# Kernel tuning notes

Measured on AMD Instinct MI355X. Metric: run time of the kernel, lower is better.

The kernel has to match this reference:

```python
import jax, jax.numpy as jnp
import numpy as np

DIM = 3456      # visual_dim
E = 1024        # embed_dim = dim_head*heads = 128*8
H = 8
D = E // H
LN_EPS = 1e-5


def _mlp(x, w1, b1, w2, b2):
    # nn.Sequential(Linear, GELU(exact), Linear)
    h = jax.nn.gelu(x @ w1.T + b1, approximate=False)
    return h @ w2.T + b2


def _ln(x, g, b):
    m = jnp.mean(x, axis=-1, keepdims=True)
    v = jnp.mean((x - m) ** 2, axis=-1, keepdims=True)
    return (x - m) * jax.lax.rsqrt(v + LN_EPS) * g + b


def setup_inputs() -> dict:
    key = jax.random.key(0)
    ks = jax.random.split(key, 24)
    std = 0.02
    d = {"x": jax.random.normal(ks[0], (5, 729, DIM), dtype=jnp.float32)}
    i = 1
    for name in ("q", "k", "v"):
        d[f"{name}_w1"] = std * jax.random.normal(ks[i], (E, DIM), dtype=jnp.float32); i += 1
        d[f"{name}_b1"] = jnp.zeros((E,), jnp.float32)
        d[f"{name}_w2"] = std * jax.random.normal(ks[i], (E, E), dtype=jnp.float32); i += 1
        d[f"{name}_b2"] = jnp.zeros((E,), jnp.float32)
        d[f"ln_{name}_g"] = jnp.ones((E,), jnp.float32)
        d[f"ln_{name}_b"] = jnp.zeros((E,), jnp.float32)
    d["in_proj_w"] = std * jax.random.normal(ks[i], (3 * E, E), dtype=jnp.float32); i += 1
    d["in_proj_b"] = jnp.zeros((3 * E,), jnp.float32)
    d["out_proj_w"] = std * jax.random.normal(ks[i], (E, E), dtype=jnp.float32); i += 1
    d["out_proj_b"] = jnp.zeros((E,), jnp.float32)
    d["to_out_w"] = std * jax.random.normal(ks[i], (DIM, E), dtype=jnp.float32)
    return d


def reference(x,
              q_w1, q_b1, q_w2, q_b2, ln_q_g, ln_q_b,
              k_w1, k_b1, k_w2, k_b2, ln_k_g, ln_k_b,
              v_w1, v_b1, v_w2, v_b2, ln_v_g, ln_v_b,
              in_proj_w, in_proj_b, out_proj_w, out_proj_b, to_out_w):
    t, hw, c = x.shape
    # spatial_temporal pattern: x_multi = x, no interpolation.
    # q/k/v: MLP -> LN -> permute(1,0,2) -> divide_feature -> flatten.
    # divide_feature is a pure permutation of tokens; all tokens end up in a
    # single (L, 1, E) attention, so full attention over the flattened
    # (hw, t) token order computes the identical result.
    q = _ln(_mlp(x, q_w1, q_b1, q_w2, q_b2), ln_q_g, ln_q_b)  # (t, hw, E)
    k = _ln(_mlp(x, k_w1, k_b1, k_w2, k_b2), ln_k_g, ln_k_b)
    v = _ln(_mlp(x, v_w1, v_b1, v_w2, v_b2), ln_v_g, ln_v_b)
    L = t * hw
    q = q.transpose(1, 0, 2).reshape(L, E)  # (hw*t, E), (h,w,t)-major order
    k = k.transpose(1, 0, 2).reshape(L, E)
    v = v.transpose(1, 0, 2).reshape(L, E)
    # nn.MultiheadAttention with packed in_proj
    qp = (q @ in_proj_w[:E].T + in_proj_b[:E]).reshape(L, H, D)
    kp = (k @ in_proj_w[E:2 * E].T + in_proj_b[E:2 * E]).reshape(L, H, D)
    vp = (v @ in_proj_w[2 * E:].T + in_proj_b[2 * E:]).reshape(L, H, D)
    scale = 1.0 / jnp.sqrt(jnp.asarray(D, q.dtype))
    scores = jnp.einsum('qhd,khd->hqk', qp, kp) * scale  # (H, L, L)
    attn = jax.nn.softmax(scores, axis=-1)
    o = jnp.einsum('hqk,khd->qhd', attn, vp).reshape(L, E)
    o = o @ out_proj_w.T + out_proj_b
    o = o.reshape(hw, t, E).transpose(1, 0, 2)  # (t, hw, E)
    out = o @ to_out_w.T                         # (t, hw, c)
    return x + out
```

## Files before the change

### kernel.cpp

```cpp
#include <hip/hip_runtime.h>
#include <hip/hip_bf16.h>

#define L_TOK 3645
#define MP    3712
#define DIMV  3456
#define EDIM  1024

typedef __attribute__((ext_vector_type(8))) short bf8;
typedef __attribute__((ext_vector_type(4))) short s4v;
typedef __attribute__((ext_vector_type(4))) float f4;

__device__ __forceinline__ short f2b(float f) {
  union { float f; unsigned u; } v; v.f = f;
  unsigned r = v.u + 0x7fffu + ((v.u >> 16) & 1u);
  return (short)(r >> 16);
}
__device__ __forceinline__ float b2f(short s) {
  union { unsigned u; float f; } v; v.u = ((unsigned)(unsigned short)s) << 16;
  return v.f;
}
__device__ __forceinline__ void gld16(const void* g, void* l) {
  __builtin_amdgcn_global_load_lds(
      (const __attribute__((address_space(1))) void*)(unsigned long long)g,
      (__attribute__((address_space(3))) void*)(unsigned)(unsigned long long)l,
      16, 0, 0);
}

struct CvtArgs {
  const float *s0, *s1, *s2, *s3, *s4, *s5, *s6, *s7;
  short *d0, *d1, *d2, *d3, *d4, *d5, *d6, *d7;
};
#define SB0 3207168
#define SB1 4091904
#define SB2 4976640
#define SB3 5861376
#define SB4 6123520
#define SB5 6385664
#define SB6 6647808
#define SB7 7532544
__global__ __launch_bounds__(256) void k_cvtall(CvtArgs a) {
  int i = blockIdx.x * 256 + threadIdx.x;
  if (i >= SB7) return;
  const float* src; short* dst; int j;
  if (i < SB0) {
    j = i; src = a.s0; dst = a.d0;
    s4v o; o[0] = 0; o[1] = 0; o[2] = 0; o[3] = 0;
    if (j < 3149280) {
      float4 v = ((const float4*)src)[j];
      o[0] = f2b(v.x); o[1] = f2b(v.y); o[2] = f2b(v.z); o[3] = f2b(v.w);
    }
    ((s4v*)dst)[j] = o;
    return;
  }
  else if (i < SB1) { j = i - SB0; src = a.s1; dst = a.d1; }
  else if (i < SB2) { j = i - SB1; src = a.s2; dst = a.d2; }
  else if (i < SB3) { j = i - SB2; src = a.s3; dst = a.d3; }
  else if (i < SB4) { j = i - SB3; src = a.s4; dst = a.d4; }
  else if (i < SB5) { j = i - SB4; src = a.s5; dst = a.d5; }
  else if (i < SB6) { j = i - SB5; src = a.s6; dst = a.d6; }
  else              { j = i - SB6; src = a.s7; dst = a.d7; }
  float4 v = ((const float4*)src)[j];
  s4v o; o[0] = f2b(v.x); o[1] = f2b(v.y); o[2] = f2b(v.z); o[3] = f2b(v.w);
  ((s4v*)dst)[j] = o;
}

__global__ __launch_bounds__(256)
void k_cvtwp(const float* __restrict__ src, short* __restrict__ dst,
             const float* __restrict__ g0, const float* __restrict__ g1,
             const float* __restrict__ g2) {
  int i = blockIdx.x * 256 + threadIdx.x;
  if (i >= 786432) return;
  int flat = i * 4;
  int k = flat & 1023;
  int z = flat >> 20;
  const float* g = (z == 0) ? g0 : (z == 1 ? g1 : g2);
  float4 v = ((const float4*)src)[i];
  float4 gv = *(const float4*)&g[k];
  s4v o; o[0] = f2b(v.x * gv.x); o[1] = f2b(v.y * gv.y);
  o[2] = f2b(v.z * gv.z); o[3] = f2b(v.w * gv.w);
  ((s4v*)dst)[i] = o;
}

__global__ __launch_bounds__(256)
void k_cvt_t(const float* __restrict__ src, short* __restrict__ dst, int n) {
  __shared__ float T[64][65];
  const int bi = blockIdx.x * 64, bj = blockIdx.y * 64;
  const int tx = threadIdx.x & 63, ty = threadIdx.x >> 6;
#pragma unroll
  for (int r = 0; r < 64; r += 4)
    T[r + ty][tx] = src[(long)(bj + r + ty) * n + bi + tx];
  __syncthreads();
#pragma unroll
  for (int r = 0; r < 64; r += 4)
    dst[(long)(bi + r + ty) * n + bj + tx] = f2b(T[tx][r + ty]);
}

__global__ __launch_bounds__(256)
void k_bvec(const float* __restrict__ wt, const float* __restrict__ opb,
            float* __restrict__ bp) {
  const int n = blockIdx.x * 4 + (threadIdx.x >> 6);
  const int lane = threadIdx.x & 63;
  const float* row = wt + (long)n * 1024;
  float s = 0.f;
  for (int k = lane * 4; k < 1024; k += 256) {
    float4 w = *(const float4*)&row[k];
    float4 b = *(const float4*)&opb[k];
    s += w.x * b.x + w.y * b.y + w.z * b.z + w.w * b.w;
  }
#pragma unroll
  for (int off = 1; off < 64; off <<= 1) s += __shfl_xor(s, off);
  if (lane == 0) bp[n] = s;
}

__global__ __launch_bounds__(256)
void k_cvec(const float* __restrict__ wp,
            const float* g0, const float* g1, const float* g2,
            const float* b0, const float* b1, const float* b2,
            const float* __restrict__ ipb,
            float* __restrict__ c1, float* __restrict__ cb2) {
  const int z = blockIdx.y;
  const int n = blockIdx.x * 4 + (threadIdx.x >> 6);
  const int lane = threadIdx.x & 63;
  const float* g  = (z == 0) ? g0 : (z == 1 ? g1 : g2);
  const float* lb = (z == 0) ? b0 : (z == 1 ? b1 : b2);
  const float* row = wp + ((long)z * 1024 + n) * 1024;
  float s1 = 0.f, s2 = 0.f;
  for (int k = lane * 4; k < 1024; k += 256) {
    float4 w = *(const float4*)&row[k];
    float4 gv = *(const float4*)&g[k];
    float4 bv = *(const float4*)&lb[k];
    s1 += w.x * gv.x + w.y * gv.y + w.z * gv.z + w.w * gv.w;
    s2 += w.x * bv.x + w.y * bv.y + w.z * bv.z + w.w * bv.w;
  }
#pragma unroll
  for (int off = 1; off < 64; off <<= 1) {
    s1 += __shfl_xor(s1, off); s2 += __shfl_xor(s2, off);
  }
  if (lane == 0) { c1[z * 1024 + n] = s1; cb2[z * 1024 + n] = s2 + ipb[z * 1024 + n]; }
}

__global__ __launch_bounds__(256)
void k_stats(const short* __restrict__ aln, float2* __restrict__ st) {
  const int z = blockIdx.y;
  const int row = blockIdx.x * 4 + (threadIdx.x >> 6);
  const int lane = threadIdx.x & 63;
  const short* a = aln + ((long)z * MP + row) * EDIM;
  float s = 0.f, q = 0.f;
  for (int k = lane * 4; k < 1024; k += 256) {
    s4v v = *(const s4v*)&a[k];
#pragma unroll
    for (int e = 0; e < 4; ++e) { float f = b2f(v[e]); s += f; q += f * f; }
  }
#pragma unroll
  for (int off = 1; off < 64; off <<= 1) {
    s += __shfl_xor(s, off); q += __shfl_xor(q, off);
  }
  if (lane == 0) {
    float m = s * (1.f / 1024.f);
    float var = q * (1.f / 1024.f) - m * m;
    float2 o; o.x = m; o.y = rsqrtf(var + 1e-5f);
    st[(long)z * MP + row] = o;
  }
}

#define GM_GELU   0
#define GM_BIAS   1
#define GM_QSCALE 2
#define GM_RESID  3
#define GM_PLAIN  4

template<int MODE>
__global__ __launch_bounds__(256)
void k_gemm(const short* __restrict__ A, long sA,
            const short* __restrict__ B, long sB,
            const float* __restrict__ bias0, const float* __restrict__ bias1,
            const float* __restrict__ bias2,
            void* __restrict__ Cout, long sC,
            int N, int K, const float* __restrict__ resid)
{
  __shared__ short As[2][128 * 32];
  __shared__ short Bs[2][128 * 32];
  const int tid  = threadIdx.x;
  const int z    = blockIdx.z;
  const int nwg  = gridDim.x * gridDim.y;
  const int orig = blockIdx.y * gridDim.x + blockIdx.x;
  const int qq   = nwg >> 3, rr = nwg & 7;
  const int xcd  = orig & 7, ofs = orig >> 3;
  const int swz  = (xcd < rr ? xcd * (qq + 1) : rr * (qq + 1) + (xcd - rr) * qq) + ofs;
  const int brow = (swz / gridDim.x) * 128;
  const int bcol = (swz % gridDim.x) * 128;

  const short* Ab = A + (long)z * sA;
  const short* Bb = B + (long)z * sB;
  const float* bias = (z == 0) ? bias0 : (z == 1 ? bias1 : bias2);

  const int wave = tid >> 6, lane = tid & 63;
  const int lg = lane >> 4, lc = lane & 15;
  const int m0 = (wave >> 1) * 64, n0 = (wave & 1) * 64;

  const int r0 = tid >> 2, seg = tid & 3;
  const int r1 = r0 + 64;
  const int so0 = (seg ^ ((r0 >> 1) & 3)) * 8;
  const int so1 = (seg ^ ((r1 >> 1) & 3)) * 8;
  const short* pA0 = Ab + (long)(brow + r0) * K + so0;
  const short* pA1 = Ab + (long)(brow + r1) * K + so1;
  const short* pB0 = Bb + (long)(bcol + r0) * K + so0;
  const short* pB1 = Bb + (long)(bcol + r1) * K + so1;

  f4 acc[4][4];
  f4 zero = {0.f, 0.f, 0.f, 0.f};
#pragma unroll
  for (int i = 0; i < 4; ++i)
#pragma unroll
    for (int j = 0; j < 4; ++j) acc[i][j] = zero;

  auto STAGE = [&](int buf) {
    gld16(pA0, &As[buf][tid * 8]);
    gld16(pA1, &As[buf][(tid + 256) * 8]);
    gld16(pB0, &Bs[buf][tid * 8]);
    gld16(pB1, &Bs[buf][(tid + 256) * 8]);
    pA0 += 32; pA1 += 32; pB0 += 32; pB1 += 32;
  };

  const int NT = K >> 5;
  STAGE(0);
  for (int t = 0; t < NT; ++t) {
    const int buf = t & 1;
    asm volatile("s_waitcnt vmcnt(0)" ::: "memory");
    __builtin_amdgcn_sched_barrier(0);
    __builtin_amdgcn_s_barrier();
    if (t + 1 < NT) STAGE((t + 1) & 1);
    const short* Al = &As[buf][0];
    const short* Bl = &Bs[buf][0];
    bf8 af[4], bfr[4];
#pragma unroll
    for (int mi = 0; mi < 4; ++mi) {
      int r = m0 + mi * 16 + lc;
      af[mi] = *(const bf8*)&Al[r * 32 + ((lg ^ ((r >> 1) & 3)) * 8)];
    }
#pragma unroll
    for (int ni = 0; ni < 4; ++ni) {
      int r = n0 + ni * 16 + lc;
      bfr[ni] = *(const bf8*)&Bl[r * 32 + ((lg ^ ((r >> 1) & 3)) * 8)];
    }
    __builtin_amdgcn_s_setprio(1);
#pragma unroll
    for (int mi = 0; mi < 4; ++mi)
#pragma unroll
      for (int ni = 0; ni < 4; ++ni)
        acc[mi][ni] = __builtin_amdgcn_mfma_f32_16x16x32_bf16(af[mi], bfr[ni], acc[mi][ni], 0, 0, 0);
    __builtin_amdgcn_s_setprio(0);
    __builtin_amdgcn_sched_barrier(0);
  }

  if (MODE == GM_RESID) {
    float* C = (float*)Cout;
#pragma unroll
    for (int ni = 0; ni < 4; ++ni) {
      int col = bcol + n0 + ni * 16 + lc;
      float bv = bias[col];
#pragma unroll
      for (int mi = 0; mi < 4; ++mi)
#pragma unroll
        for (int r = 0; r < 4; ++r) {
          int row = brow + m0 + mi * 16 + lg * 4 + r;
          if (row < L_TOK)
            C[(long)row * N + col] = acc[mi][ni][r] + bv + resid[(long)row * N + col];
        }
    }
  } else {
    short* C = (short*)Cout + (long)z * sC;
    const float alpha = (MODE == GM_QSCALE && z == 0) ? 0.08838834764831845f : 1.0f;
#pragma unroll
    for (int ni = 0; ni < 4; ++ni) {
      int col = bcol + n0 + ni * 16 + lc;
      float bv = 0.f;
      if (MODE != GM_PLAIN) bv = bias[col];
#pragma unroll
      for (int mi = 0; mi < 4; ++mi)
#pragma unroll
        for (int r = 0; r < 4; ++r) {
          int row = brow + m0 + mi * 16 + lg * 4 + r;
          float v = acc[mi][ni][r] + bv;
          if (MODE == GM_GELU) v = 0.5f * v * (1.f + erff(v * 0.70710678118654752f));
          v *= alpha;
          C[(long)row * EDIM + col] = f2b(v);
        }
    }
  }
}

__global__ __launch_bounds__(256)
void k_gemmln(const short* __restrict__ A, long sA,
              const short* __restrict__ B, long sB,
              const float2* __restrict__ st,
              const float* __restrict__ c1, const float* __restrict__ cb2,
              short* __restrict__ Cout, long sC)
{
  __shared__ short As[2][128 * 32];
  __shared__ short Bs[2][128 * 32];
  const int tid  = threadIdx.x;
  const int z    = blockIdx.z;
  const int K    = EDIM;
  const int nwg  = gridDim.x * gridDim.y;
  const int orig = blockIdx.y * gridDim.x + blockIdx.x;
  const int qq   = nwg >> 3, rr = nwg & 7;
  const int xcd  = orig & 7, ofs = orig >> 3;
  const int swz  = (xcd < rr ? xcd * (qq + 1) : rr * (qq + 1) + (xcd - rr) * qq) + ofs;
  const int brow = (swz / gridDim.x) * 128;
  const int bcol = (swz % gridDim.x) * 128;

  const short* Ab = A + (long)z * sA;
  const short* Bb = B + (long)z * sB;

  const int wave = tid >> 6, lane = tid & 63;
  const int lg = lane >> 4, lc = lane & 15;
  const int m0 = (wave >> 1) * 64, n0 = (wave & 1) * 64;

  const int r0 = tid >> 2, seg = tid & 3;
  const int r1 = r0 + 64;
  const int so0 = (seg ^ ((r0 >> 1) & 3)) * 8;
  const int so1 = (seg ^ ((r1 >> 1) & 3)) * 8;
  const short* pA0 = Ab + (long)(brow + r0) * K + so0;
  const short* pA1 = Ab + (long)(brow + r1) * K + so1;
  const short* pB0 = Bb + (long)(bcol + r0) * K + so0;
  const short* pB1 = Bb + (long)(bcol + r1) * K + so1;

  f4 acc[4][4];
  f4 zero = {0.f, 0.f, 0.f, 0.f};
#pragma unroll
  for (int i = 0; i < 4; ++i)
#pragma unroll
    for (int j = 0; j < 4; ++j) acc[i][j] = zero;

  auto STAGE = [&](int buf) {
    gld16(pA0, &As[buf][tid * 8]);
    gld16(pA1, &As[buf][(tid + 256) * 8]);
    gld16(pB0, &Bs[buf][tid * 8]);
    gld16(pB1, &Bs[buf][(tid + 256) * 8]);
    pA0 += 32; pA1 += 32; pB0 += 32; pB1 += 32;
  };

  const int NT = K >> 5;
  STAGE(0);
  for (int t = 0; t < NT; ++t) {
    const int buf = t & 1;
    asm volatile("s_waitcnt vmcnt(0)" ::: "memory");
    __builtin_amdgcn_sched_barrier(0);
    __builtin_amdgcn_s_barrier();
    if (t + 1 < NT) STAGE((t + 1) & 1);
    const short* Al = &As[buf][0];
    const short* Bl = &Bs[buf][0];
    bf8 af[4], bfr[4];
#pragma unroll
    for (int mi = 0; mi < 4; ++mi) {
      int r = m0 + mi * 16 + lc;
      af[mi] = *(const bf8*)&Al[r * 32 + ((lg ^ ((r >> 1) & 3)) * 8)];
    }
#pragma unroll
    for (int ni = 0; ni < 4; ++ni) {
      int r = n0 + ni * 16 + lc;
      bfr[ni] = *(const bf8*)&Bl[r * 32 + ((lg ^ ((r >> 1) & 3)) * 8)];
    }
    __builtin_amdgcn_s_setprio(1);
#pragma unroll
    for (int mi = 0; mi < 4; ++mi)
#pragma unroll
      for (int ni = 0; ni < 4; ++ni)
        acc[mi][ni] = __builtin_amdgcn_mfma_f32_16x16x32_bf16(af[mi], bfr[ni], acc[mi][ni], 0, 0, 0);
    __builtin_amdgcn_s_setprio(0);
    __builtin_amdgcn_sched_barrier(0);
  }

  short* C = Cout + (long)z * sC;
  const float alpha = (z == 0) ? 0.08838834764831845f : 1.0f;
  float2 sv[4][4];
#pragma unroll
  for (int mi = 0; mi < 4; ++mi)
#pragma unroll
    for (int r = 0; r < 4; ++r)
      sv[mi][r] = st[(long)z * MP + brow + m0 + mi * 16 + lg * 4 + r];
#pragma unroll
  for (int ni = 0; ni < 4; ++ni) {
    int col = bcol + n0 + ni * 16 + lc;
    float c1v = c1[z * 1024 + col];
    float cbv = cb2[z * 1024 + col];
#pragma unroll
    for (int mi = 0; mi < 4; ++mi)
#pragma unroll
      for (int r = 0; r < 4; ++r) {
        int row = brow + m0 + mi * 16 + lg * 4 + r;
        float v = sv[mi][r].y * (acc[mi][ni][r] - sv[mi][r].x * c1v) + cbv;
        C[(long)row * EDIM + col] = f2b(v * alpha);
      }
  }
}

__global__ __launch_bounds__(256)
void k_vtrans(const short* __restrict__ vp, short* __restrict__ vpT)
{
  const int kb = blockIdx.x * 64, h = blockIdx.y;
  __shared__ short T[64 * 128];
  const int tid = threadIdx.x;
#pragma unroll
  for (int i = 0; i < 4; ++i) {
    int c = tid + 256 * i;
    int r = c >> 4, x = c & 15;
    bf8 val = *(const bf8*)&vp[(long)(kb + r) * EDIM + h * 128 + x * 8];
    *(bf8*)&T[r * 128 + ((x ^ (r & 7)) * 8)] = val;
  }
  __syncthreads();
#pragma unroll
  for (int i = 0; i < 4; ++i) {
    int c = tid + 256 * i;
    int dr = c >> 3, x = c & 7;
    short tmp[8];
#pragma unroll
    for (int e = 0; e < 8; ++e) {
      int kv = x * 8 + e;
      tmp[e] = T[kv * 128 + (((dr >> 3) ^ (kv & 7)) << 3) + (dr & 7)];
    }
    *(bf8*)&vpT[((long)h * 128 + dr) * MP + kb + x * 8] = *(bf8*)tmp;
  }
}

__global__ __launch_bounds__(256)
void k_attn(const short* __restrict__ qp, const short* __restrict__ kp,
            const short* __restrict__ vpT,
            short* __restrict__ op0, short* __restrict__ op1,
            float* __restrict__ lsums)
{
  const int bx = blockIdx.x;
  const int h = bx & 7;
  const int t2 = bx >> 3;
  const int qi = t2 % 29, sp = t2 / 29;
  const int qb = qi * 128;
  short* opart = sp ? op1 : op0;
  const int t0 = sp ? 29 : 0, t1 = sp ? 57 : 29;

  const int tid = threadIdx.x, wave = tid >> 6, lane = tid & 63;
  const int lg = lane >> 4, lc = lane & 15;
  __shared__ short Ks[2][64 * 128];
  __shared__ short Vs[2][128 * 64];
  __shared__ short Ps[4][32 * 64];

  const int q0 = qb + wave * 32;
  bf8 qf[2][4];
#pragma unroll
  for (int g = 0; g < 2; ++g)
#pragma unroll
    for (int d4 = 0; d4 < 4; ++d4)
      qf[g][d4] = *(const bf8*)&qp[(long)(q0 + g * 16 + lc) * EDIM + h * 128 + d4 * 32 + lg * 8];

  f4 oacc[2][8];
  f4 zero = {0.f, 0.f, 0.f, 0.f};
#pragma unroll
  for (int g = 0; g < 2; ++g)
#pragma unroll
    for (int dt = 0; dt < 8; ++dt) oacc[g][dt] = zero;
  float lsum0 = 0.f, lsum1 = 0.f;

  auto STAGE = [&](short* ksb, short* vsb, int kb) {
#pragma unroll
    for (int i = 0; i < 4; ++i) {
      int c = tid + 256 * i; int r = c >> 4, x = c & 15;
      gld16(&kp[(long)(kb + r) * EDIM + h * 128 + (x ^ (r & 7)) * 8], &ksb[c * 8]);
    }
#pragma unroll
    for (int i = 0; i < 4; ++i) {
      int c = tid + 256 * i; int dr = c >> 3, x = c & 7;
      gld16(&vpT[((long)h * 128 + dr) * MP + kb + (x ^ (dr & 7)) * 8], &vsb[c * 8]);
    }
  };

  STAGE(Ks[t0 & 1], Vs[t0 & 1], t0 * 64);

  for (int t = t0; t < t1; ++t) {
    const int kb = t * 64;
    const short* ksb = Ks[t & 1];
    const short* vsb = Vs[t & 1];
    __builtin_amdgcn_s_barrier();
    if (t + 1 < t1) {
      STAGE(Ks[(t + 1) & 1], Vs[(t + 1) & 1], kb + 64);
      asm volatile("s_waitcnt vmcnt(8)" ::: "memory");
    } else {
      asm volatile("s_waitcnt vmcnt(0)" ::: "memory");
    }
    __builtin_amdgcn_sched_barrier(0);
    __builtin_amdgcn_s_barrier();
    __builtin_amdgcn_sched_barrier(0);

#pragma unroll
    for (int s = 0; s < 4; ++s) {
      const int krow = s * 16 + lc;
      bf8 kf[4];
#pragma unroll
      for (int d4 = 0; d4 < 4; ++d4)
        kf[d4] = *(const bf8*)&ksb[krow * 128 + (((d4 * 4 + lg) ^ (krow & 7)) * 8)];
      f4 sa0 = zero, sa1 = zero;
      __builtin_amdgcn_s_setprio(1);
#pragma unroll
      for (int d4 = 0; d4 < 4; ++d4) {
        sa0 = __builtin_amdgcn_mfma_f32_16x16x32_bf16(kf[d4], qf[0][d4], sa0, 0, 0, 0);
        sa1 = __builtin_amdgcn_mfma_f32_16x16x32_bf16(kf[d4], qf[1][d4], sa1, 0, 0, 0);
      }
      __builtin_amdgcn_s_setprio(0);
      const int kvb = kb + s * 16 + lg * 4;
#pragma unroll
      for (int g = 0; g < 2; ++g) {
        f4 sa = g ? sa1 : sa0;
        float p[4];
#pragma unroll
        for (int r = 0; r < 4; ++r) {
          float e = __expf(sa[r]);
          p[r] = (kvb + r < L_TOK) ? e : 0.f;
          if (g) lsum1 += p[r]; else lsum0 += p[r];
        }
        s4v pk; pk[0] = f2b(p[0]); pk[1] = f2b(p[1]); pk[2] = f2b(p[2]); pk[3] = f2b(p[3]);
        *(s4v*)&Ps[wave][(g * 16 + lc) * 64 + ((s * 16 + lg * 4) ^ ((lc & 7) << 3))] = pk;
      }
    }
    bf8 pf[2][2];
#pragma unroll
    for (int g = 0; g < 2; ++g) {
      pf[g][0] = *(const bf8*)&Ps[wave][(g * 16 + lc) * 64 + ((lg * 8) ^ ((lc & 7) << 3))];
      pf[g][1] = *(const bf8*)&Ps[wave][(g * 16 + lc) * 64 + ((32 + lg * 8) ^ ((lc & 7) << 3))];
    }
#pragma unroll
    for (int dt = 0; dt < 8; ++dt) {
      const int vrow = dt * 16 + lc;
      bf8 vf0 = *(const bf8*)&vsb[vrow * 64 + ((lg ^ (vrow & 7)) * 8)];
      bf8 vf1 = *(const bf8*)&vsb[vrow * 64 + (((4 + lg) ^ (vrow & 7)) * 8)];
      __builtin_amdgcn_s_setprio(1);
      oacc[0][dt] = __builtin_amdgcn_mfma_f32_16x16x32_bf16(pf[0][0], vf0, oacc[0][dt], 0, 0, 0);
      oacc[0][dt] = __builtin_amdgcn_mfma_f32_16x16x32_bf16(pf[0][1], vf1, oacc[0][dt], 0, 0, 0);
      oacc[1][dt] = __builtin_amdgcn_mfma_f32_16x16x32_bf16(pf[1][0], vf0, oacc[1][dt], 0, 0, 0);
      oacc[1][dt] = __builtin_amdgcn_mfma_f32_16x16x32_bf16(pf[1][1], vf1, oacc[1][dt], 0, 0, 0);
      __builtin_amdgcn_s_setprio(0);
    }
    __builtin_amdgcn_sched_barrier(0);
  }

  lsum0 += __shfl_xor(lsum0, 16);
  lsum0 += __shfl_xor(lsum0, 32);
  lsum1 += __shfl_xor(lsum1, 16);
  lsum1 += __shfl_xor(lsum1, 32);
  if (lg == 0) {
    lsums[((sp * 8) + h) * MP + q0 + lc]      = lsum0;
    lsums[((sp * 8) + h) * MP + q0 + 16 + lc] = lsum1;
  }
#pragma unroll
  for (int g = 0; g < 2; ++g)
#pragma unroll
    for (int dt = 0; dt < 8; ++dt)
#pragma unroll
      for (int r = 0; r < 4; ++r) {
        int orow = q0 + g * 16 + lg * 4 + r;
        opart[(long)orow * EDIM + h * 128 + dt * 16 + lc] = f2b(oacc[g][dt][r]);
      }
}

__global__ __launch_bounds__(256)
void k_comb(const short* __restrict__ p0, const short* __restrict__ p1,
            const float* __restrict__ ls, short* __restrict__ ob)
{
  int i = blockIdx.x * 256 + threadIdx.x;
  int q = i >> 7;
  int h = (i & 127) >> 4;
  float rinv = 1.f / (ls[h * MP + q] + ls[(8 + h) * MP + q]);
  bf8 a = ((const bf8*)p0)[i];
  bf8 b = ((const bf8*)p1)[i];
  bf8 o;
#pragma unroll
  for (int j = 0; j < 8; ++j) o[j] = f2b((b2f(a[j]) + b2f(b[j])) * rinv);
  ((bf8*)ob)[i] = o;
}

extern "C" void kernel_launch(void* const* d_in, const int* in_sizes, int n_in,
                              void* d_out, int out_size, void* d_ws, size_t ws_size,
                              hipStream_t stream)
{
  const float* x   = (const float*)d_in[0];
  const float* ipb = (const float*)d_in[20];
  const float* opb = (const float*)d_in[22];

  char* ws = (char*)d_ws;
  short*  xb     = (short*)(ws + 0);
  short*  aln    = (short*)(ws + 0);
  short*  pt0    = (short*)(ws + 0);
  short*  pt1    = (short*)(ws + 7602176);
  float*  lsums  = (float*)(ws + 15204352);
  short*  ob     = (short*)(ws + 15466496);
  float2* stats  = (float2*)(ws + 23068672);
  float*  bp     = (float*)(ws + 23330816);
  float*  c1     = (float*)(ws + 23461888);
  float*  cb2    = (float*)(ws + 23592960);
  short*  h1     = (short*)(ws + 25657344);
  short*  proj   = (short*)(ws + 25657344);
  short*  w1b    = (short*)(ws + 48463872);
  short*  wprime = w1b;
  short*  w2b    = (short*)(ws + 69697536);
  short*  wpb    = (short*)(ws + 75988992);
  short*  woT    = (short*)(ws + 82280448);
  short*  wtb    = (short*)(ws + 84377600);
  short*  vpT    = (short*)(ws + 91455488);

  CvtArgs ca;
  ca.s0 = x;                      ca.d0 = xb;
  ca.s1 = (const float*)d_in[1];  ca.d1 = w1b;
  ca.s2 = (const float*)d_in[7];  ca.d2 = w1b + 3538944;
  ca.s3 = (const float*)d_in[13]; ca.d3 = w1b + 7077888;
  ca.s4 = (const float*)d_in[3];  ca.d4 = w2b;
  ca.s5 = (const float*)d_in[9];  ca.d5 = w2b + 1048576;
  ca.s6 = (const float*)d_in[15]; ca.d6 = w2b + 2097152;
  ca.s7 = (const float*)d_in[23]; ca.d7 = wtb;
  k_cvtall<<<(SB7 + 255) / 256, 256, 0, stream>>>(ca);
  k_cvtwp<<<3072, 256, 0, stream>>>((const float*)d_in[19], wpb,
      (const float*)d_in[5], (const float*)d_in[11], (const float*)d_in[17]);
  dim3 gct(16, 16);
  k_cvt_t<<<gct, 256, 0, stream>>>((const float*)d_in[21], woT, 1024);

  dim3 g3(8, 29, 3);
  k_gemm<GM_GELU><<<g3, 256, 0, stream>>>(xb, 0, w1b, 3538944,
      (const float*)d_in[2], (const float*)d_in[8], (const float*)d_in[14],
      h1, (long)MP * EDIM, EDIM, DIMV, nullptr);
  k_bvec<<<864, 256, 0, stream>>>((const float*)d_in[23], opb, bp);
  dim3 gcv(256, 3);
  k_cvec<<<gcv, 256, 0, stream>>>((const float*)d_in[19],
      (const float*)d_in[5], (const float*)d_in[11], (const float*)d_in[17],
      (const float*)d_in[6], (const float*)d_in[12], (const float*)d_in[18],
      ipb, c1, cb2);
  dim3 gwp(8, 27, 1);
  k_gemm<GM_PLAIN><<<gwp, 256, 0, stream>>>(wtb, 0, woT, 0,
      nullptr, nullptr, nullptr, wprime, 0, EDIM, EDIM, nullptr);
  k_gemm<GM_BIAS><<<g3, 256, 0, stream>>>(h1, (long)MP * EDIM, w2b, 1048576,
      (const float*)d_in[4], (const float*)d_in[10], (const float*)d_in[16],
      aln, (long)MP * EDIM, EDIM, EDIM, nullptr);
  dim3 gst(MP / 4, 3);
  k_stats<<<gst, 256, 0, stream>>>(aln, stats);
  k_gemmln<<<g3, 256, 0, stream>>>(aln, (long)MP * EDIM, wpb, 1048576,
      stats, c1, cb2, proj, (long)MP * EDIM);
  dim3 gt(MP / 64, 8);
  k_vtrans<<<gt, 256, 0, stream>>>(proj + 2L * MP * EDIM, vpT);
  k_attn<<<29 * 2 * 8, 256, 0, stream>>>(proj, proj + (long)MP * EDIM, vpT,
      pt0, pt1, lsums);
  k_comb<<<(MP * EDIM / 8) / 256, 256, 0, stream>>>(pt0, pt1, lsums, ob);
  dim3 g5(27, 29, 1);
  k_gemm<GM_RESID><<<g5, 256, 0, stream>>>(ob, 0, wprime, 0,
      bp, bp, bp, d_out, 0, DIMV, EDIM, x);
}
```

Baseline: 409.7 us.

## Fuse the three first-layer MLP GEMMs so each block reuses one A tile

Replaces the z-batched first MLP GEMM (q/k/v each reading x separately) with a single kernel where every block loads its x tile once and multiplies it against all three weight matrices, keeping three sets of accumulators. This cuts global and LDS traffic for A by a factor of three and launches 232 blocks instead of 696. The cost is 192 accumulator registers per thread and a larger LDS footprint, which forces one block per CU and lowers occupancy. The grid also becomes much smaller relative to the CU count.

```diff
diff --git a/kernel.cpp b/kernel.cpp
--- a/kernel.cpp
+++ b/kernel.cpp
@@ -169,6 +169,117 @@
 #define GM_RESID  3
 #define GM_PLAIN  4
 
+__global__ __launch_bounds__(256, 1)
+void k_gemm1f(const short* __restrict__ A, const short* __restrict__ B, long sB,
+              const float* __restrict__ bias0, const float* __restrict__ bias1,
+              const float* __restrict__ bias2,
+              short* __restrict__ Cout, long sC, int K)
+{
+  __shared__ short As[2][128 * 32];
+  __shared__ short Bs[3][2][128 * 32];
+  const int tid  = threadIdx.x;
+  const int nwg  = gridDim.x * gridDim.y;
+  const int orig = blockIdx.y * gridDim.x + blockIdx.x;
+  const int qq   = nwg >> 3, rr = nwg & 7;
+  const int xcd  = orig & 7, ofs = orig >> 3;
+  const int swz  = (xcd < rr ? xcd * (qq + 1) : rr * (qq + 1) + (xcd - rr) * qq) + ofs;
+  const int brow = (swz / gridDim.x) * 128;
+  const int bcol = (swz % gridDim.x) * 128;
+
+  const int wave = tid >> 6, lane = tid & 63;
+  const int lg = lane >> 4, lc = lane & 15;
+  const int m0 = (wave >> 1) * 64, n0 = (wave & 1) * 64;
+
+  const int r0 = tid >> 2, seg = tid & 3;
+  const int r1 = r0 + 64;
+  const int so0 = (seg ^ ((r0 >> 1) & 3)) * 8;
+  const int so1 = (seg ^ ((r1 >> 1) & 3)) * 8;
+  const short* pA0 = A + (long)(brow + r0) * K + so0;
+  const short* pA1 = A + (long)(brow + r1) * K + so1;
+  const short* pB0[3];
+  const short* pB1[3];
+#pragma unroll
+  for (int z = 0; z < 3; ++z) {
+    pB0[z] = B + (long)z * sB + (long)(bcol + r0) * K + so0;
+    pB1[z] = B + (long)z * sB + (long)(bcol + r1) * K + so1;
+  }
+
+  f4 acc[3][4][4];
+  f4 zero = {0.f, 0.f, 0.f, 0.f};
+#pragma unroll
+  for (int z = 0; z < 3; ++z)
+#pragma unroll
+    for (int i = 0; i < 4; ++i)
+#pragma unroll
+      for (int j = 0; j < 4; ++j) acc[z][i][j] = zero;
+
+  auto STAGE = [&](int buf) {
+    gld16(pA0, &As[buf][tid * 8]);         pA0 += 32;
+    gld16(pA1, &As[buf][(tid + 256) * 8]); pA1 += 32;
+#pragma unroll
+    for (int z = 0; z < 3; ++z) {
+      gld16(pB0[z], &Bs[z][buf][tid * 8]);         pB0[z] += 32;
+      gld16(pB1[z], &Bs[z][buf][(tid + 256) * 8]); pB1[z] += 32;
+    }
+  };
+
+  const int NT = K >> 5;
+  STAGE(0);
+  for (int t = 0; t < NT; ++t) {
+    const int buf = t & 1;
+    asm volatile("s_waitcnt vmcnt(0)" ::: "memory");
+    __builtin_amdgcn_sched_barrier(0);
+    __builtin_amdgcn_s_barrier();
+    if (t + 1 < NT) STAGE((t + 1) & 1);
+
+    const short* Al = &As[buf][0];
+    bf8 af[4];
+#pragma unroll
+    for (int mi = 0; mi < 4; ++mi) {
+      int r = m0 + mi * 16 + lc;
+      af[mi] = *(const bf8*)&Al[r * 32 + ((lg ^ ((r >> 1) & 3)) * 8)];
+    }
+#pragma unroll
+    for (int z = 0; z < 3; ++z) {
+      const short* Bl = &Bs[z][buf][0];
+      bf8 bfr[4];
+#pragma unroll
+      for (int ni = 0; ni < 4; ++ni) {
+        int r = n0 + ni * 16 + lc;
+        bfr[ni] = *(const bf8*)&Bl[r * 32 + ((lg ^ ((r >> 1) & 3)) * 8)];
+      }
+      __builtin_amdgcn_s_setprio(1);
+#pragma unroll
+      for (int mi = 0; mi < 4; ++mi)
+#pragma unroll
+        for (int ni = 0; ni < 4; ++ni)
+          acc[z][mi][ni] = __builtin_amdgcn_mfma_f32_16x16x32_bf16(af[mi], bfr[ni], acc[z][mi][ni], 0, 0, 0);
+      __builtin_amdgcn_s_setprio(0);
+    }
+    __builtin_amdgcn_sched_barrier(0);
+  }
+
+#pragma unroll
+  for (int z = 0; z < 3; ++z) {
+    const float* bias = (z == 0) ? bias0 : (z == 1 ? bias1 : bias2);
+    short* C = Cout + (long)z * sC;
+#pragma unroll
+    for (int ni = 0; ni < 4; ++ni) {
+      int col = bcol + n0 + ni * 16 + lc;
+      float bv = bias[col];
+#pragma unroll
+      for (int mi = 0; mi < 4; ++mi)
+#pragma unroll
+        for (int r = 0; r < 4; ++r) {
+          int row = brow + m0 + mi * 16 + lg * 4 + r;
+          float v = acc[z][mi][ni][r] + bv;
+          v = 0.5f * v * (1.f + erff(v * 0.70710678118654752f));
+          C[(long)row * EDIM + col] = f2b(v);
+        }
+    }
+  }
+}
+
 template<int MODE>
 __global__ __launch_bounds__(256)
 void k_gemm(const short* __restrict__ A, long sA,
@@ -620,10 +731,10 @@
   dim3 gct(16, 16);
   k_cvt_t<<<gct, 256, 0, stream>>>((const float*)d_in[21], woT, 1024);
 
-  dim3 g3(8, 29, 3);
-  k_gemm<GM_GELU><<<g3, 256, 0, stream>>>(xb, 0, w1b, 3538944,
+  dim3 g1f(8, 29);
+  k_gemm1f<<<g1f, 256, 0, stream>>>(xb, w1b, 3538944,
       (const float*)d_in[2], (const float*)d_in[8], (const float*)d_in[14],
-      h1, (long)MP * EDIM, EDIM, DIMV, nullptr);
+      h1, (long)MP * EDIM, DIMV);
   k_bvec<<<864, 256, 0, stream>>>((const float*)d_in[23], opb, bp);
   dim3 gcv(256, 3);
   k_cvec<<<gcv, 256, 0, stream>>>((const float*)d_in[19],
@@ -633,6 +744,7 @@
   dim3 gwp(8, 27, 1);
   k_gemm<GM_PLAIN><<<gwp, 256, 0, stream>>>(wtb, 0, woT, 0,
       nullptr, nullptr, nullptr, wprime, 0, EDIM, EDIM, nullptr);
+  dim3 g3(8, 29, 3);
   k_gemm<GM_BIAS><<<g3, 256, 0, stream>>>(h1, (long)MP * EDIM, w2b, 1048576,
       (const float*)d_in[4], (const float*)d_in[10], (const float*)d_in[16],
       aln, (long)MP * EDIM, EDIM, EDIM, nullptr);
```

Result: slower. 433.5 us (+5.8%).

## Split attention KV range four ways with register-staged single-buffered K/V tiles

Applied to the files above, without the earlier changes.

The attention kernel now splits the key range into four chunks instead of two, launching twice as many blocks, and the combine kernel sums four partial outputs and four row sums. The LDS double buffer filled by direct global-to-LDS loads is replaced with a single K/V buffer that is filled from registers prefetched one tile ahead, and launch bounds request three blocks per SM. The aim is better occupancy and more parallelism across the 256 CUs for a short attention sequence. The cost is extra partial-output traffic in the combine step, more registers held for prefetch, and a barrier-heavy single-buffer pipeline.

```diff
diff --git a/kernel.cpp b/kernel.cpp
--- a/kernel.cpp
+++ b/kernel.cpp
@@ -424,10 +424,11 @@
   }
 }
 
-__global__ __launch_bounds__(256)
+__global__ __launch_bounds__(256, 3)
 void k_attn(const short* __restrict__ qp, const short* __restrict__ kp,
             const short* __restrict__ vpT,
             short* __restrict__ op0, short* __restrict__ op1,
+            short* __restrict__ op2, short* __restrict__ op3,
             float* __restrict__ lsums)
 {
   const int bx = blockIdx.x;
@@ -435,13 +436,14 @@
   const int t2 = bx >> 3;
   const int qi = t2 % 29, sp = t2 / 29;
   const int qb = qi * 128;
-  short* opart = sp ? op1 : op0;
-  const int t0 = sp ? 29 : 0, t1 = sp ? 57 : 29;
+  short* opart = (sp == 0) ? op0 : (sp == 1) ? op1 : (sp == 2) ? op2 : op3;
+  const int t0 = (sp == 0) ? 0  : (sp == 1) ? 15 : (sp == 2) ? 29 : 43;
+  const int t1 = (sp == 0) ? 15 : (sp == 1) ? 29 : (sp == 2) ? 43 : 57;
 
   const int tid = threadIdx.x, wave = tid >> 6, lane = tid & 63;
   const int lg = lane >> 4, lc = lane & 15;
-  __shared__ short Ks[2][64 * 128];
-  __shared__ short Vs[2][128 * 64];
+  __shared__ short Ks[64 * 128];
+  __shared__ short Vs[128 * 64];
   __shared__ short Ps[4][32 * 64];
 
   const int q0 = qb + wave * 32;
@@ -460,32 +462,33 @@
     for (int dt = 0; dt < 8; ++dt) oacc[g][dt] = zero;
   float lsum0 = 0.f, lsum1 = 0.f;
 
-  auto STAGE = [&](short* ksb, short* vsb, int kb) {
+  bf8 rK[4], rV[4];
+  auto LOADREG = [&](int kb) {
 #pragma unroll
     for (int i = 0; i < 4; ++i) {
       int c = tid + 256 * i; int r = c >> 4, x = c & 15;
-      gld16(&kp[(long)(kb + r) * EDIM + h * 128 + (x ^ (r & 7)) * 8], &ksb[c * 8]);
+      rK[i] = *(const bf8*)&kp[(long)(kb + r) * EDIM + h * 128 + (x ^ (r & 7)) * 8];
     }
 #pragma unroll
     for (int i = 0; i < 4; ++i) {
       int c = tid + 256 * i; int dr = c >> 3, x = c & 7;
-      gld16(&vpT[((long)h * 128 + dr) * MP + kb + (x ^ (dr & 7)) * 8], &vsb[c * 8]);
+      rV[i] = *(const bf8*)&vpT[((long)h * 128 + dr) * MP + kb + (x ^ (dr & 7)) * 8];
     }
   };
 
-  STAGE(Ks[t0 & 1], Vs[t0 & 1], t0 * 64);
+  LOADREG(t0 * 64);
 
   for (int t = t0; t < t1; ++t) {
     const int kb = t * 64;
-    const short* ksb = Ks[t & 1];
-    const short* vsb = Vs[t & 1];
     __builtin_amdgcn_s_barrier();
-    if (t + 1 < t1) {
-      STAGE(Ks[(t + 1) & 1], Vs[(t + 1) & 1], kb + 64);
-      asm volatile("s_waitcnt vmcnt(8)" ::: "memory");
-    } else {
-      asm volatile("s_waitcnt vmcnt(0)" ::: "memory");
-    }
+    asm volatile("s_waitcnt vmcnt(0)" ::: "memory");
+    __builtin_amdgcn_sched_barrier(0);
+#pragma unroll
+    for (int i = 0; i < 4; ++i) *(bf8*)&Ks[(tid + 256 * i) * 8] = rK[i];
+#pragma unroll
+    for (int i = 0; i < 4; ++i) *(bf8*)&Vs[(tid + 256 * i) * 8] = rV[i];
+    if (t + 1 < t1) LOADREG(kb + 64);
+    asm volatile("s_waitcnt lgkmcnt(0)" ::: "memory");
     __builtin_amdgcn_sched_barrier(0);
     __builtin_amdgcn_s_barrier();
     __builtin_amdgcn_sched_barrier(0);
@@ -496,7 +499,7 @@
       bf8 kf[4];
 #pragma unroll
       for (int d4 = 0; d4 < 4; ++d4)
-        kf[d4] = *(const bf8*)&ksb[krow * 128 + (((d4 * 4 + lg) ^ (krow & 7)) * 8)];
+        kf[d4] = *(const bf8*)&Ks[krow * 128 + (((d4 * 4 + lg) ^ (krow & 7)) * 8)];
       f4 sa0 = zero, sa1 = zero;
       __builtin_amdgcn_s_setprio(1);
 #pragma unroll
@@ -529,8 +532,8 @@
 #pragma unroll
     for (int dt = 0; dt < 8; ++dt) {
       const int vrow = dt * 16 + lc;
-      bf8 vf0 = *(const bf8*)&vsb[vrow * 64 + ((lg ^ (vrow & 7)) * 8)];
-      bf8 vf1 = *(const bf8*)&vsb[vrow * 64 + (((4 + lg) ^ (vrow & 7)) * 8)];
+      bf8 vf0 = *(const bf8*)&Vs[vrow * 64 + ((lg ^ (vrow & 7)) * 8)];
+      bf8 vf1 = *(const bf8*)&Vs[vrow * 64 + (((4 + lg) ^ (vrow & 7)) * 8)];
       __builtin_amdgcn_s_setprio(1);
       oacc[0][dt] = __builtin_amdgcn_mfma_f32_16x16x32_bf16(pf[0][0], vf0, oacc[0][dt], 0, 0, 0);
       oacc[0][dt] = __builtin_amdgcn_mfma_f32_16x16x32_bf16(pf[0][1], vf1, oacc[0][dt], 0, 0, 0);
@@ -562,17 +565,22 @@
 
 __global__ __launch_bounds__(256)
 void k_comb(const short* __restrict__ p0, const short* __restrict__ p1,
+            const short* __restrict__ p2, const short* __restrict__ p3,
             const float* __restrict__ ls, short* __restrict__ ob)
 {
   int i = blockIdx.x * 256 + threadIdx.x;
   int q = i >> 7;
   int h = (i & 127) >> 4;
-  float rinv = 1.f / (ls[h * MP + q] + ls[(8 + h) * MP + q]);
+  float rinv = 1.f / (ls[h * MP + q] + ls[(8 + h) * MP + q] +
+                      ls[(16 + h) * MP + q] + ls[(24 + h) * MP + q]);
   bf8 a = ((const bf8*)p0)[i];
   bf8 b = ((const bf8*)p1)[i];
+  bf8 c = ((const bf8*)p2)[i];
+  bf8 d = ((const bf8*)p3)[i];
   bf8 o;
 #pragma unroll
-  for (int j = 0; j < 8; ++j) o[j] = f2b((b2f(a[j]) + b2f(b[j])) * rinv);
+  for (int j = 0; j < 8; ++j)
+    o[j] = f2b((b2f(a[j]) + b2f(b[j]) + b2f(c[j]) + b2f(d[j])) * rinv);
   ((bf8*)ob)[i] = o;
 }
 
@@ -589,16 +597,18 @@
   short*  aln    = (short*)(ws + 0);
   short*  pt0    = (short*)(ws + 0);
   short*  pt1    = (short*)(ws + 7602176);
-  float*  lsums  = (float*)(ws + 15204352);
   short*  ob     = (short*)(ws + 15466496);
   float2* stats  = (float2*)(ws + 23068672);
   float*  bp     = (float*)(ws + 23330816);
   float*  c1     = (float*)(ws + 23461888);
   float*  cb2    = (float*)(ws + 23592960);
+  float*  lsums  = (float*)(ws + 23605248);
   short*  h1     = (short*)(ws + 25657344);
   short*  proj   = (short*)(ws + 25657344);
   short*  w1b    = (short*)(ws + 48463872);
   short*  wprime = w1b;
+  short*  pt2    = (short*)(ws + 55541760);
+  short*  pt3    = (short*)(ws + 63143936);
   short*  w2b    = (short*)(ws + 69697536);
   short*  wpb    = (short*)(ws + 75988992);
   short*  woT    = (short*)(ws + 82280448);
@@ -642,9 +652,9 @@
       stats, c1, cb2, proj, (long)MP * EDIM);
   dim3 gt(MP / 64, 8);
   k_vtrans<<<gt, 256, 0, stream>>>(proj + 2L * MP * EDIM, vpT);
-  k_attn<<<29 * 2 * 8, 256, 0, stream>>>(proj, proj + (long)MP * EDIM, vpT,
-      pt0, pt1, lsums);
-  k_comb<<<(MP * EDIM / 8) / 256, 256, 0, stream>>>(pt0, pt1, lsums, ob);
+  k_attn<<<29 * 4 * 8, 256, 0, stream>>>(proj, proj + (long)MP * EDIM, vpT,
+      pt0, pt1, pt2, pt3, lsums);
+  k_comb<<<(MP * EDIM / 8) / 256, 256, 0, stream>>>(pt0, pt1, pt2, pt3, lsums, ob);
   dim3 g5(27, 29, 1);
   k_gemm<GM_RESID><<<g5, 256, 0, stream>>>(ob, 0, wprime, 0,
       bp, bp, bp, d_out, 0, DIMV, EDIM, x);
```

Result: slower. 595.2 us (+45.3%).
